# Kernel tuning notes

Measured on AMD Instinct MI355X. Metric: run time of the kernel, lower is better.

## Reference

```python
import jax, jax.numpy as jnp
import numpy as np

N = 200000   # total atoms in batched graph
E = 3200000  # total bonds (directed edges)
B = 512      # number of graphs / sequences
L = 1000     # miRNA sequence length


def _gcn(x, W, b, src, dst, dis):
    # PyG GCNConv: add self-loops, symmetric normalization D^-1/2 A D^-1/2
    h = x @ W                                   # [N, Fout]
    msg = (dis[src] * dis[dst])[:, None] * h[src]
    agg = jax.ops.segment_sum(msg, dst, num_segments=x.shape[0])
    return agg + (dis * dis)[:, None] * h + b   # self-loop term + bias


def _conv1d(x, k, b):
    # x: [B, C, L], k: [O, I, K]  (torch Conv1d, VALID padding)
    y = jax.lax.conv_general_dilated(x, k, (1,), 'VALID',
                                     dimension_numbers=('NCH', 'OIH', 'NCH'))
    return y + b[None, :, None]


def _mp3(x):
    # torch MaxPool1d(3): window 3, stride 3, floor
    return jax.lax.reduce_window(x, -jnp.inf, jax.lax.max, (1, 1, 3), (1, 1, 3), 'VALID')


def setup_inputs() -> dict:
    key = jax.random.key(0)
    ks = jax.random.split(key, 24)
    w = lambda k, s: (jax.random.normal(k, s, jnp.float32) * 0.1)
    p = {}
    p['x'] = jax.random.normal(ks[0], (N, 4), jnp.float32)
    p['edge_index'] = jax.random.randint(ks[1], (2, E), 0, N, jnp.int32)
    p['batch'] = (jnp.arange(N, dtype=jnp.int32) * B // N).astype(jnp.int32)  # every graph non-empty
    p['target'] = jax.random.normal(ks[2], (B, L, 5), jnp.float32)
    # GCN layers 4->4->8->16
    p['W1'] = w(ks[3], (4, 4));    p['b1'] = jnp.zeros(4, jnp.float32)
    p['W2'] = w(ks[4], (4, 8));    p['b2'] = jnp.zeros(8, jnp.float32)
    p['W3'] = w(ks[5], (8, 16));   p['b3'] = jnp.zeros(16, jnp.float32)
    p['Wg1'] = w(ks[6], (16, 1024)); p['bg1'] = jnp.zeros(1024, jnp.float32)
    p['Wg2'] = w(ks[7], (1024, 128)); p['bg2'] = jnp.zeros(128, jnp.float32)
    # CNN stack on sequences, kernels [O, I, 8]
    p['K1'] = w(ks[8], (32, 5, 8));   p['cb1'] = jnp.zeros(32, jnp.float32)
    p['K2'] = w(ks[9], (64, 32, 8));  p['cb2'] = jnp.zeros(64, jnp.float32)
    p['K3'] = w(ks[10], (128, 64, 8)); p['cb3'] = jnp.zeros(128, jnp.float32)
    p['Wxt'] = w(ks[11], (128, 128)); p['bxt'] = jnp.zeros(128, jnp.float32)
    # fusion head
    p['Wf1'] = w(ks[12], (256, 1024)); p['bf1'] = jnp.zeros(1024, jnp.float32)
    p['Wf2'] = w(ks[13], (1024, 512)); p['bf2'] = jnp.zeros(512, jnp.float32)
    p['Wo'] = w(ks[14], (512, 2));     p['bo'] = jnp.zeros(2, jnp.float32)
    return p


def reference(x, edge_index, batch, target, W1, b1, W2, b2, W3, b3,
              Wg1, bg1, Wg2, bg2, K1, cb1, K2, cb2, K3, cb3,
              Wxt, bxt, Wf1, bf1, Wf2, bf2, Wo, bo):
    src, dst = edge_index[0], edge_index[1]
    deg = jax.ops.segment_sum(jnp.ones(src.shape[0], x.dtype), dst,
                              num_segments=x.shape[0]) + 1.0  # +1 self-loop
    dis = jax.lax.rsqrt(deg)
    # Graph branch (dropout is identity in eval)
    h = jax.nn.relu(_gcn(x, W1, b1, src, dst, dis))
    h = jax.nn.relu(_gcn(h, W2, b2, src, dst, dis))
    h = jax.nn.relu(_gcn(h, W3, b3, src, dst, dis))
    g = jax.ops.segment_max(h, batch, num_segments=B)  # global_max_pool
    g = jax.nn.relu(g @ Wg1 + bg1)
    g = g @ Wg2 + bg2
    # Sequence branch
    t = jnp.transpose(target, (0, 2, 1))  # [B, 5, L]
    c = _mp3(jax.nn.relu(_conv1d(t, K1, cb1)))
    c = _mp3(jax.nn.relu(_conv1d(c, K2, cb2)))
    c = _mp3(jax.nn.relu(_conv1d(c, K3, cb3)))
    c = jnp.mean(c, axis=2)               # [B, 128]
    c = jax.nn.relu(c @ Wxt + bxt)
    # Fusion head
    xc = jnp.concatenate([g, c], axis=1)  # [B, 256]
    xc = jax.nn.relu(xc @ Wf1 + bf1)
    xc = jax.nn.relu(xc @ Wf2 + bf2)
    return xc @ Wo + bo                    # [B, 2]
```

## Files before the change

### kernel.cpp

```cpp
#include <hip/hip_runtime.h>
#include <hip/hip_fp16.h>
#include <cstddef>

#define NA 200000
#define NE 3200000
#define NB 512
#define NBKT 256
#define BKTN 782
#define BKTCAP 16384
#define NEPB 3200

typedef _Float16 hv2 __attribute__((ext_vector_type(2)));
typedef _Float16 half8 __attribute__((ext_vector_type(8)));
typedef float floatx4 __attribute__((ext_vector_type(4)));
union UH2 { unsigned u; __half2 h; hv2 v; };
__device__ __forceinline__ float4 h4f(unsigned a, unsigned b) {
    UH2 x, y; x.u = a; y.u = b;
    float2 fa = __half22float2(x.h), fb = __half22float2(y.h);
    return make_float4(fa.x, fa.y, fb.x, fb.y);
}
__device__ __forceinline__ unsigned f2h(float a, float b) {
    UH2 r; r.h = __float22half2_rn(make_float2(a, b));
    return r.u;
}

__global__ void k_init(unsigned* g, int* gcursor,
                       float* gvec, const float* __restrict__ bg2,
                       float* xf2, const float* __restrict__ bf2,
                       float* xf1, const float* __restrict__ bf1,
                       const float* __restrict__ K2, const float* __restrict__ K3,
                       __half* __restrict__ Wt2, __half* __restrict__ Wt3) {
    int i = blockIdx.x * blockDim.x + threadIdx.x;
    if (i < NB * 16) g[i] = 0u;
    if (i < NBKT) gcursor[i] = i * BKTCAP;
    if (i < NB * 128) gvec[i] = bg2[i & 127];
    if (i < NB * 512) xf2[i] = bf2[i & 511];
    if (i < NB * 1024) xf1[i] = bf1[i & 1023];
    if (i < 64 * 32 * 8) {
        int o = i >> 8, rem = i & 255, c = rem >> 3, kk = rem & 7;
        Wt2[(o << 8) + (kk << 5) + c] = __float2half(K2[i]);
    }
    if (i < 128 * 64 * 8) {
        int o = i >> 9, rem = i & 511, c = rem >> 3, kk = rem & 7;
        Wt3[(o << 9) + (kk << 6) + c] = __float2half(K3[i]);
    }
}

template<int CIN, int COUT, int OBLK, int LIN, int PITCH, int POUT, int NTT>
__device__ __forceinline__ void dev_conv1(int b, int oy,
        const float* __restrict__ in, const float* __restrict__ Kw,
        const float* __restrict__ bias, __half* __restrict__ out,
        float* s_in) {
    constexpr int SPO = 256 / OBLK;
    constexpr int PT = (NTT < 4) ? NTT : 4;
    constexpr int NPASS = (NTT + PT - 1) / PT;
    for (int idx = threadIdx.x; idx < CIN * PITCH; idx += 256) s_in[idx] = 0.f;
    __syncthreads();
    for (int idx = threadIdx.x; idx < LIN * CIN; idx += 256) {
        int p = idx / CIN, c = idx - p * CIN;
        s_in[c * PITCH + p] = in[(size_t)b * (LIN * CIN) + idx];
    }
    __syncthreads();
    int ol = threadIdx.x / SPO;
    int s  = threadIdx.x - ol * SPO;
    int o  = oy * OBLK + ol;
    float bo = bias[o];
    const float* wrow = Kw + (size_t)o * CIN * 8;
    for (int pass = 0; pass < NPASS; pass++) {
        float acc[PT][12];
#pragma unroll
        for (int tt = 0; tt < PT; tt++)
#pragma unroll
            for (int j = 0; j < 12; j++) acc[tt][j] = 0.f;
        bool vld[PT]; int tgs[PT];
#pragma unroll
        for (int tt = 0; tt < PT; tt++) {
            int ta = pass * PT + tt;
            int tg = s + SPO * ta;
            tgs[tt] = tg;
            vld[tt] = (ta < NTT) && (4 * tg < POUT);
        }
        for (int i = 0; i < CIN; i++) {
            float wa[8];
            const float4* wp = (const float4*)(wrow + (size_t)i * 8);
            *(float4*)&wa[0] = wp[0];
            *(float4*)&wa[4] = wp[1];
#pragma unroll
            for (int tt = 0; tt < PT; tt++) {
                if (vld[tt]) {
                    const float4* xr = (const float4*)&s_in[i * PITCH + 12 * tgs[tt]];
                    float xa[20];
#pragma unroll
                    for (int q = 0; q < 5; q++) *(float4*)&xa[4 * q] = xr[q];
#pragma unroll
                    for (int j = 0; j < 12; j++) {
                        float sm = acc[tt][j];
#pragma unroll
                        for (int k = 0; k < 8; k++) sm = fmaf(xa[j + k], wa[k], sm);
                        acc[tt][j] = sm;
                    }
                }
            }
        }
#pragma unroll
        for (int tt = 0; tt < PT; tt++) {
            if (vld[tt]) {
#pragma unroll
                for (int p = 0; p < 4; p++) {
                    int P = 4 * tgs[tt] + p;
                    if (P < POUT) {
                        float m = fmaxf(fmaxf(acc[tt][3 * p], acc[tt][3 * p + 1]), acc[tt][3 * p + 2]);
                        out[((size_t)b * COUT + o) * POUT + P] = __float2half(fmaxf(m + bo, 0.f));
                    }
                }
            }
        }
    }
}

__device__ __forceinline__ void dev_conv2_mfma(int b,
        const __half* __restrict__ pool1, const __half* __restrict__ Wt2,
        const float* __restrict__ cb2, __half* __restrict__ pool2t,
        char* smem) {
    __half* sT   = (__half*)smem;
    __half* outS = (__half*)smem;
    const __half* inp = pool1 + (size_t)b * (32 * 331);
    for (int idx = threadIdx.x; idx < 32 * 331; idx += 256) {
        int c = idx / 331;
        int p = idx - c * 331;
        sT[p * 40 + c] = inp[idx];
    }
    __syncthreads();
    int lane = threadIdx.x & 63, wv = threadIdx.x >> 6;
    int l15 = lane & 15, lg = lane >> 4;
    int mtBeg = wv * 5;
    int nmt = (wv == 3) ? 6 : 5;
    const floatx4 FZ = {0.f, 0.f, 0.f, 0.f};
    floatx4 acc[6][4];
#pragma unroll
    for (int mi = 0; mi < 6; mi++)
#pragma unroll
        for (int nt = 0; nt < 4; nt++) acc[mi][nt] = FZ;
    const half8* WB = (const half8*)Wt2;
    for (int s = 0; s < 8; s++) {
        half8 bfr[4];
#pragma unroll
        for (int nt = 0; nt < 4; nt++)
            bfr[nt] = WB[(nt * 16 + l15) * 32 + s * 4 + lg];
        half8 afr[6];
#pragma unroll
        for (int mi = 0; mi < 6; mi++) {
            if (mi < nmt) {
                int row = (mtBeg + mi) * 16 + l15 + s;
                afr[mi] = *(const half8*)(sT + row * 40 + lg * 8);
            }
        }
#pragma unroll
        for (int mi = 0; mi < 6; mi++) {
            if (mi < nmt) {
#pragma unroll
                for (int nt = 0; nt < 4; nt++)
                    acc[mi][nt] = __builtin_amdgcn_mfma_f32_16x16x32_f16(
                        afr[mi], bfr[nt], acc[mi][nt], 0, 0, 0);
            }
        }
    }
    __syncthreads();
    float bo[4];
#pragma unroll
    for (int nt = 0; nt < 4; nt++) bo[nt] = cb2[nt * 16 + l15];
    __half* op = pool2t + (size_t)b * (108 * 64);
    for (int h = 0; h < 2; h++) {
        int r0 = h * 168;
#pragma unroll
        for (int mi = 0; mi < 6; mi++) {
            if (mi < nmt) {
#pragma unroll
                for (int nt = 0; nt < 4; nt++) {
                    int o = nt * 16 + l15;
#pragma unroll
                    for (int r = 0; r < 4; r++) {
                        int p = (mtBeg + mi) * 16 + lg * 4 + r;
                        unsigned pl = (unsigned)(p - r0);
                        if (pl < 168u) {
                            float v = fmaxf(acc[mi][nt][r] + bo[nt], 0.f);
                            outS[pl * 68 + o] = __float2half(v);
                        }
                    }
                }
            }
        }
        __syncthreads();
        int nP = h ? 52 : 56;
        for (int idx = threadIdx.x; idx < nP * 64; idx += 256) {
            int Pl = idx >> 6, o = idx & 63;
            int P = h * 56 + Pl;
            int p = 3 * P - r0;
            float v0 = __half2float(outS[p * 68 + o]);
            float v1 = __half2float(outS[(p + 1) * 68 + o]);
            float v2 = __half2float(outS[(p + 2) * 68 + o]);
            op[P * 64 + o] = __float2half(fmaxf(fmaxf(v0, v1), v2));
        }
        __syncthreads();
    }
}

__device__ __forceinline__ void dev_conv3_mfma(int b,
        const __half* __restrict__ pool2t, const __half* __restrict__ Wt3,
        const float* __restrict__ cb3, float* __restrict__ pool3,
        char* smem) {
    __half* sT  = (__half*)smem;
    float* outS = (float*)smem;
    const uint4* inp = (const uint4*)(pool2t + (size_t)b * (108 * 64));
    for (int t = threadIdx.x; t < 108 * 8; t += 256) {
        int r = t >> 3, s8 = t & 7;
        *(uint4*)(sT + r * 72 + s8 * 8) = inp[t];
    }
    __syncthreads();
    int lane = threadIdx.x & 63, wv = threadIdx.x >> 6;
    int l15 = lane & 15, lg = lane >> 4;
    int mtBeg = wv * 2;
    int nmt = (wv == 3) ? 1 : 2;
    const floatx4 FZ = {0.f, 0.f, 0.f, 0.f};
    floatx4 acc[2][8];
#pragma unroll
    for (int mi = 0; mi < 2; mi++)
#pragma unroll
        for (int nt = 0; nt < 8; nt++) acc[mi][nt] = FZ;
    const half8* WB = (const half8*)Wt3;
    for (int s = 0; s < 16; s++) {
        half8 bfr[8];
#pragma unroll
        for (int nt = 0; nt < 8; nt++)
            bfr[nt] = WB[(nt * 16 + l15) * 64 + s * 4 + lg];
        half8 afr[2];
#pragma unroll
        for (int mi = 0; mi < 2; mi++) {
            if (mi < nmt) {
                int row = (mtBeg + mi) * 16 + l15 + (s >> 1);
                afr[mi] = *(const half8*)(sT + row * 72 + (s & 1) * 32 + lg * 8);
            }
        }
#pragma unroll
        for (int mi = 0; mi < 2; mi++) {
            if (mi < nmt) {
#pragma unroll
                for (int nt = 0; nt < 8; nt++)
                    acc[mi][nt] = __builtin_amdgcn_mfma_f32_16x16x32_f16(
                        afr[mi], bfr[nt], acc[mi][nt], 0, 0, 0);
            }
        }
    }
    __syncthreads();
    float bo[8];
#pragma unroll
    for (int nt = 0; nt < 8; nt++) bo[nt] = cb3[nt * 16 + l15];
    float* op = pool3 + (size_t)b * (128 * 33);
    for (int pp = 0; pp < 3; pp++) {
        int t0 = 3 * pp;
#pragma unroll
        for (int mi = 0; mi < 2; mi++) {
            int tile = mtBeg + mi;
            if (mi < nmt && tile >= t0 && tile < t0 + 3) {
#pragma unroll
                for (int nt = 0; nt < 8; nt++) {
                    int o = nt * 16 + l15;
#pragma unroll
                    for (int r = 0; r < 4; r++) {
                        int p = tile * 16 + lg * 4 + r;
                        if (p < 100)
                            outS[(p - 48 * pp) * 132 + o] =
                                fmaxf(acc[mi][nt][r] + bo[nt], 0.f);
                    }
                }
            }
        }
        __syncthreads();
        int nP = (pp == 2) ? 1 : 16;
        for (int idx = threadIdx.x; idx < nP * 128; idx += 256) {
            int Pl = idx >> 7, o = idx & 127;
            int P = 16 * pp + Pl;
            int p = 3 * P - 48 * pp;
            float v0 = outS[p * 132 + o];
            float v1 = outS[(p + 1) * 132 + o];
            float v2 = outS[(p + 2) * 132 + o];
            op[o * 33 + P] = fmaxf(fmaxf(v0, v1), v2);
        }
        __syncthreads();
    }
}

__global__ __launch_bounds__(256) void k_A(
        const int* __restrict__ src, const int* __restrict__ dst,
        int* __restrict__ gcursor, unsigned* __restrict__ stage,
        const float* __restrict__ tgt, const float* __restrict__ K1,
        const float* __restrict__ cb1, __half* __restrict__ pool1) {
    __shared__ __align__(16) char smem[20160];
    int bx = blockIdx.x;
    if (bx >= 1000) {
        dev_conv1<5, 32, 16, 1000, 1008, 331, 6>(bx - 1000, 0, tgt, K1, cb1,
                                                 pool1, (float*)smem);
        return;
    }
    int* hcnt  = (int*)smem;
    int* hbase = hcnt + 256;
    int* lbase = hbase + 256;
    unsigned* sbuf = (unsigned*)(lbase + 256);
    unsigned char* sbkt = (unsigned char*)(sbuf + NEPB);
    int t = threadIdx.x;
    int e0 = bx * NEPB;
    hcnt[t] = 0;
    __syncthreads();
    const int4* d4 = (const int4*)(dst + e0);
    for (int i = t; i < NEPB / 4; i += 256) {
        int4 d = d4[i];
        atomicAdd(&hcnt[d.x / BKTN], 1);
        atomicAdd(&hcnt[d.y / BKTN], 1);
        atomicAdd(&hcnt[d.z / BKTN], 1);
        atomicAdd(&hcnt[d.w / BKTN], 1);
    }
    __syncthreads();
    int myc = hcnt[t];
    hbase[t] = atomicAdd(&gcursor[t], myc);
    __syncthreads();
#pragma unroll
    for (int off = 1; off < 256; off <<= 1) {
        int u = (t >= off) ? hcnt[t - off] : 0;
        __syncthreads();
        hcnt[t] += u;
        __syncthreads();
    }
    lbase[t] = hcnt[t] - myc;
    hcnt[t] = 0;
    __syncthreads();
    const int4* s4 = (const int4*)(src + e0);
    for (int i = t; i < NEPB / 4; i += 256) {
        int4 d = d4[i];
        int4 s = s4[i];
        int ds[4] = {d.x, d.y, d.z, d.w};
        int ss[4] = {s.x, s.y, s.z, s.w};
#pragma unroll
        for (int j = 0; j < 4; j++) {
            int bkt = ds[j] / BKTN;
            int dloc = ds[j] - bkt * BKTN;
            int k = atomicAdd(&hcnt[bkt], 1);
            int pos = lbase[bkt] + k;
            sbuf[pos] = ((unsigned)dloc << 18) | (unsigned)ss[j];
            sbkt[pos] = (unsigned char)bkt;
        }
    }
    __syncthreads();
    for (int i = t; i < NEPB; i += 256) {
        unsigned v = sbuf[i];
        int bkt = sbkt[i];
        stage[hbase[bkt] + (i - lbase[bkt])] = v;
    }
}

__global__ __launch_bounds__(256) void k_Bp(
        const unsigned* __restrict__ stage, const int* __restrict__ gcursor,
        int* __restrict__ rowptr, int* __restrict__ cnt, int* __restrict__ csr,
        const float* __restrict__ x, float4* __restrict__ dt1,
        const float* __restrict__ tgt, const float* __restrict__ K1,
        const float* __restrict__ cb1, __half* __restrict__ pool1) {
    __shared__ __align__(16) char smem[20160];
    __shared__ int sbase;
    int bx = blockIdx.x;
    if (bx >= NBKT) {
        dev_conv1<5, 32, 16, 1000, 1008, 331, 6>(bx - NBKT, 1, tgt, K1, cb1,
                                                 pool1, (float*)smem);
        return;
    }
    int* lcnt    = (int*)smem;
    int* lpos    = lcnt + BKTN;
    int* partial = lpos + BKTN;
    int t = threadIdx.x;
    int bkt = bx;
    int tot = gcursor[t] - t * BKTCAP;
    partial[t] = tot;
    __syncthreads();
#pragma unroll
    for (int off = 1; off < 256; off <<= 1) {
        int u = (t >= off) ? partial[t - off] : 0;
        __syncthreads();
        partial[t] += u;
        __syncthreads();
    }
    if (t == 0) sbase = (bkt == 0) ? 0 : partial[bkt - 1];
    __syncthreads();
    int base = sbase;
    int n0 = bkt * BKTN;
    int ncnt = (NA - n0 < BKTN) ? (NA - n0) : BKTN;
    int eBeg = bkt * BKTCAP;
    int eCnt = gcursor[bkt] - eBeg;
    for (int i = t; i < BKTN; i += 256) lcnt[i] = 0;
    __syncthreads();
    for (int i = t; i < eCnt; i += 256)
        atomicAdd(&lcnt[stage[eBeg + i] >> 18], 1);
    __syncthreads();
    int mysum = 0;
#pragma unroll
    for (int j = 0; j < 4; j++) {
        int node = 4 * t + j;
        if (node < ncnt) mysum += lcnt[node];
    }
    partial[t] = mysum;
    __syncthreads();
#pragma unroll
    for (int off = 1; off < 256; off <<= 1) {
        int u = (t >= off) ? partial[t - off] : 0;
        __syncthreads();
        partial[t] += u;
        __syncthreads();
    }
    int running = partial[t] - mysum;
#pragma unroll
    for (int j = 0; j < 4; j++) {
        int node = 4 * t + j;
        if (node < ncnt) {
            lpos[node] = running;
            rowptr[n0 + node] = base + running;
            cnt[n0 + node] = lcnt[node];
            running += lcnt[node];
        }
    }
    __syncthreads();
    for (int i = t; i < eCnt; i += 256) {
        unsigned v = stage[eBeg + i];
        int dloc = v >> 18;
        int s = v & 0x3FFFF;
        int k = atomicAdd(&lpos[dloc], 1);
        csr[base + k] = s;
    }
    for (int i = t; i < ncnt; i += 256) {
        int n = n0 + i;
        float4 p = ((const float4*)x)[n];
        float dv = rsqrtf((float)lcnt[i] + 1.0f);
        dt1[n] = make_float4(dv * p.x, dv * p.y, dv * p.z, dv * p.w);
    }
}

__global__ __launch_bounds__(256) void k_B(
        const __half* __restrict__ pool1, const __half* __restrict__ Wt2,
        const float* __restrict__ cb2, __half* __restrict__ pool2t,
        const float4* __restrict__ dt1, const int* __restrict__ rowptr,
        const int* __restrict__ cnt, const int* __restrict__ csr,
        const float* __restrict__ W1, const float* __restrict__ b1,
        float4* __restrict__ dt2) {
    __shared__ __align__(16) char smem[27520];
    int bx = blockIdx.x;
    if (bx < 512) {
        dev_conv2_mfma(bx, pool1, Wt2, cb2, pool2t, smem);
        return;
    }
    __shared__ float sW[16];
    if (threadIdx.x < 16) sW[threadIdx.x] = W1[threadIdx.x];
    __syncthreads();
    int n = (bx - 512) * 256 + threadIdx.x;
    if (n >= NA) return;
    int cn = cnt[n];
    float dv = rsqrtf((float)cn + 1.0f);
    const int* row = csr + rowptr[n];
    float4 acc = dt1[n];
    int e = 0;
    for (; e + 7 < cn; e += 8) {
        int idx[8];
#pragma unroll
        for (int u = 0; u < 8; u++) idx[u] = row[e + u];
        float4 v[8];
#pragma unroll
        for (int u = 0; u < 8; u++) v[u] = dt1[idx[u]];
#pragma unroll
        for (int u = 0; u < 8; u++) {
            acc.x += v[u].x; acc.y += v[u].y; acc.z += v[u].z; acc.w += v[u].w;
        }
    }
    for (; e < cn; e++) {
        float4 v = dt1[row[e]];
        acc.x += v.x; acc.y += v.y; acc.z += v.z; acc.w += v.w;
    }
    const float4 bq = *(const float4*)b1;
    float a[4] = {acc.x, acc.y, acc.z, acc.w};
    float bb[4] = {bq.x, bq.y, bq.z, bq.w};
    float o[4];
#pragma unroll
    for (int f = 0; f < 4; f++) {
        float s = 0.f;
#pragma unroll
        for (int k = 0; k < 4; k++) s = fmaf(a[k], sW[k * 4 + f], s);
        o[f] = dv * fmaxf(fmaf(dv, s, bb[f]), 0.f);
    }
    dt2[n] = make_float4(o[0], o[1], o[2], o[3]);
}

__global__ __launch_bounds__(256) void k_C(
        const __half* __restrict__ pool2t, const __half* __restrict__ Wt3,
        const float* __restrict__ cb3, float* __restrict__ pool3,
        const float4* __restrict__ dt2, const int* __restrict__ rowptr,
        const int* __restrict__ cnt, const int* __restrict__ csr,
        const float* __restrict__ W2, const float* __restrict__ b2,
        uint4* __restrict__ dt3) {
    __shared__ __align__(16) char smem[25344];
    int bx = blockIdx.x;
    if (bx < 512) {
        dev_conv3_mfma(bx, pool2t, Wt3, cb3, pool3, smem);
        return;
    }
    __shared__ float sW[32];
    if (threadIdx.x < 32) sW[threadIdx.x] = W2[threadIdx.x];
    __syncthreads();
    int n = (bx - 512) * 256 + threadIdx.x;
    if (n >= NA) return;
    int cn = cnt[n];
    float dv = rsqrtf((float)cn + 1.0f);
    const int* row = csr + rowptr[n];
    float4 acc = dt2[n];
    int e = 0;
    for (; e + 7 < cn; e += 8) {
        int idx[8];
#pragma unroll
        for (int u = 0; u < 8; u++) idx[u] = row[e + u];
        float4 v[8];
#pragma unroll
        for (int u = 0; u < 8; u++) v[u] = dt2[idx[u]];
#pragma unroll
        for (int u = 0; u < 8; u++) {
            acc.x += v[u].x; acc.y += v[u].y; acc.z += v[u].z; acc.w += v[u].w;
        }
    }
    for (; e < cn; e++) {
        float4 v = dt2[row[e]];
        acc.x += v.x; acc.y += v.y; acc.z += v.z; acc.w += v.w;
    }
    float a[4] = {acc.x, acc.y, acc.z, acc.w};
    float o[8];
#pragma unroll
    for (int f = 0; f < 8; f++) {
        float s = 0.f;
#pragma unroll
        for (int k = 0; k < 4; k++) s = fmaf(a[k], sW[k * 8 + f], s);
        o[f] = dv * fmaxf(fmaf(dv, s, b2[f]), 0.f);
    }
    dt3[n] = make_uint4(f2h(o[0], o[1]), f2h(o[2], o[3]),
                        f2h(o[4], o[5]), f2h(o[6], o[7]));
}

__global__ __launch_bounds__(256) void k_D(
        const uint4* __restrict__ dt3, const int* __restrict__ rowptr,
        const int* __restrict__ cnt, const int* __restrict__ csr,
        const float* __restrict__ W3, const float* __restrict__ b3,
        const int* __restrict__ batch, unsigned* __restrict__ g,
        const float* __restrict__ pool3, const float* __restrict__ Wxt,
        const float* __restrict__ bxt, float* __restrict__ cx) {
    int bx = blockIdx.x;
    if (bx >= 782) {
        __shared__ float sa[8 * 128];
        int b0 = (bx - 782) * 8;
        for (int t = threadIdx.x; t < 8 * 128; t += 256) {
            int gg = t >> 7, k = t & 127;
            const float* r = pool3 + ((size_t)(b0 + gg) * 128 + k) * 33;
            float s = 0.f;
#pragma unroll
            for (int p = 0; p < 33; p++) s += r[p];
            sa[t] = s * (1.f / 33.f);
        }
        __syncthreads();
        int j = threadIdx.x;
        if (j >= 128) return;
        float bj = bxt[j];
        float acc[8];
#pragma unroll
        for (int gg = 0; gg < 8; gg++) acc[gg] = bj;
#pragma unroll 4
        for (int k = 0; k < 128; k++) {
            float w = Wxt[(size_t)k * 128 + j];
#pragma unroll
            for (int gg = 0; gg < 8; gg++) acc[gg] = fmaf(sa[gg * 128 + k], w, acc[gg]);
        }
#pragma unroll
        for (int gg = 0; gg < 8; gg++)
            cx[(size_t)(b0 + gg) * 128 + j] = fmaxf(acc[gg], 0.f);
        return;
    }
    __shared__ float sW[128];
    __shared__ unsigned sg[32];
    __shared__ int sbmin;
    int id = bx;
    if (threadIdx.x < 128) sW[threadIdx.x] = W3[threadIdx.x];
    if (threadIdx.x < 32) sg[threadIdx.x] = 0u;
    if (threadIdx.x == 0) sbmin = batch[id * 256];
    __syncthreads();
    int n = id * 256 + threadIdx.x;
    if (n < NA) {
        int cn = cnt[n];
        float dv = rsqrtf((float)cn + 1.0f);
        const int* row = csr + rowptr[n];
        uint4 sv = dt3[n];
        float4 lo = h4f(sv.x, sv.y), hi = h4f(sv.z, sv.w);
        float a0 = lo.x, a1 = lo.y, a2 = lo.z, a3 = lo.w;
        float a4 = hi.x, a5 = hi.y, a6 = hi.z, a7 = hi.w;
        int e = 0;
        for (; e + 3 < cn; e += 4) {
            uint4 p0 = dt3[row[e]],     p1 = dt3[row[e + 1]];
            uint4 p2 = dt3[row[e + 2]], p3 = dt3[row[e + 3]];
            float4 l0 = h4f(p0.x, p0.y), h0 = h4f(p0.z, p0.w);
            float4 l1 = h4f(p1.x, p1.y), h1 = h4f(p1.z, p1.w);
            float4 l2 = h4f(p2.x, p2.y), h2 = h4f(p2.z, p2.w);
            float4 l3 = h4f(p3.x, p3.y), h3v = h4f(p3.z, p3.w);
            a0 += (l0.x + l1.x) + (l2.x + l3.x);
            a1 += (l0.y + l1.y) + (l2.y + l3.y);
            a2 += (l0.z + l1.z) + (l2.z + l3.z);
            a3 += (l0.w + l1.w) + (l2.w + l3.w);
            a4 += (h0.x + h1.x) + (h2.x + h3v.x);
            a5 += (h0.y + h1.y) + (h2.y + h3v.y);
            a6 += (h0.z + h1.z) + (h2.z + h3v.z);
            a7 += (h0.w + h1.w) + (h2.w + h3v.w);
        }
        for (; e < cn; e++) {
            uint4 p = dt3[row[e]];
            float4 l = h4f(p.x, p.y), h = h4f(p.z, p.w);
            a0 += l.x; a1 += l.y; a2 += l.z; a3 += l.w;
            a4 += h.x; a5 += h.y; a6 += h.z; a7 += h.w;
        }
        float af[8] = {a0, a1, a2, a3, a4, a5, a6, a7};
        int rb = batch[n] - sbmin;
        if (rb > 1) rb = 1;
#pragma unroll
        for (int f = 0; f < 16; f++) {
            float s = 0.f;
#pragma unroll
            for (int k = 0; k < 8; k++) s = fmaf(af[k], sW[k * 16 + f], s);
            float r = fmaxf(fmaf(dv, s, b3[f]), 0.f);
            atomicMax(&sg[rb * 16 + f], __float_as_uint(r));
        }
    }
    __syncthreads();
    if (threadIdx.x < 32) {
        unsigned v = sg[threadIdx.x];
        int rb2 = threadIdx.x >> 4, f = threadIdx.x & 15;
        int bbn = sbmin + rb2;
        if (v != 0u && bbn < NB) atomicMax(&g[bbn * 16 + f], v);
    }
}

__global__ __launch_bounds__(256) void k_head_g(
        const float* __restrict__ g, const float* __restrict__ Wg1,
        const float* __restrict__ bg1, float* __restrict__ gp1) {
    __shared__ float sa[8 * 16];
    int bx = blockIdx.x;
    int b0 = (bx >> 2) * 8;
    if (threadIdx.x < 128)
        sa[threadIdx.x] = g[b0 * 16 + threadIdx.x];
    __syncthreads();
    int j = (bx & 3) * 256 + threadIdx.x;
    float bj = bg1[j];
    float acc[8];
#pragma unroll
    for (int gg = 0; gg < 8; gg++) acc[gg] = bj;
#pragma unroll
    for (int k = 0; k < 16; k++) {
        float w = Wg1[(size_t)k * 1024 + j];
#pragma unroll
        for (int gg = 0; gg < 8; gg++) acc[gg] = fmaf(sa[gg * 16 + k], w, acc[gg]);
    }
#pragma unroll
    for (int gg = 0; gg < 8; gg++)
        gp1[(size_t)(b0 + gg) * 1024 + j] = fmaxf(acc[gg], 0.f);
}

__global__ __launch_bounds__(256) void k_gvec_ks(
        const float* __restrict__ gp1, const float* __restrict__ Wg2,
        float* __restrict__ gvec) {
    __shared__ float sa[8 * 128];
    int k0 = blockIdx.x * 128;
    int b0 = blockIdx.y * 8;
    for (int t = threadIdx.x; t < 8 * 128; t += 256) {
        int gg = t >> 7, k = t & 127;
        sa[t] = gp1[(size_t)(b0 + gg) * 1024 + k0 + k];
    }
    __syncthreads();
    int j  = threadIdx.x & 127;
    int kh = (threadIdx.x >> 7) * 64;
    const float* Wp = Wg2 + (size_t)(k0 + kh) * 128 + j;
    float acc[8];
#pragma unroll
    for (int gg = 0; gg < 8; gg++) acc[gg] = 0.f;
    for (int k = 0; k < 64; k += 16) {
        float w[16];
#pragma unroll
        for (int u = 0; u < 16; u++) w[u] = Wp[(size_t)(k + u) * 128];
#pragma unroll
        for (int u = 0; u < 16; u++) {
#pragma unroll
            for (int gg = 0; gg < 8; gg++)
                acc[gg] = fmaf(sa[gg * 128 + kh + k + u], w[u], acc[gg]);
        }
    }
#pragma unroll
    for (int gg = 0; gg < 8; gg++)
        atomicAdd(&gvec[(size_t)(b0 + gg) * 128 + j], acc[gg]);
}

__global__ __launch_bounds__(256) void k_cat2(
        const float* __restrict__ gvec, const float* __restrict__ cx,
        const float* __restrict__ Wf1, float* __restrict__ xf1) {
    __shared__ float sa[8 * 128];
    int jx = blockIdx.x & 3;
    int kh = blockIdx.x >> 2;
    int b0 = blockIdx.y * 8;
    const float* A = kh ? cx : gvec;
    for (int t = threadIdx.x; t < 8 * 128; t += 256) {
        int gg = t >> 7, k = t & 127;
        sa[t] = A[(size_t)(b0 + gg) * 128 + k];
    }
    __syncthreads();
    int j = jx * 256 + threadIdx.x;
    const float* Wp = Wf1 + (size_t)(kh * 128) * 1024 + j;
    float acc[8];
#pragma unroll
    for (int gg = 0; gg < 8; gg++) acc[gg] = 0.f;
    for (int k = 0; k < 128; k += 16) {
        float w[16];
#pragma unroll
        for (int u = 0; u < 16; u++) w[u] = Wp[(size_t)(k + u) * 1024];
#pragma unroll
        for (int u = 0; u < 16; u++) {
#pragma unroll
            for (int gg = 0; gg < 8; gg++)
                acc[gg] = fmaf(sa[gg * 128 + k + u], w[u], acc[gg]);
        }
    }
#pragma unroll
    for (int gg = 0; gg < 8; gg++)
        atomicAdd(&xf1[(size_t)(b0 + gg) * 1024 + j], acc[gg]);
}

__global__ __launch_bounds__(256) void k_xf2_ks(
        const float* __restrict__ xf1, const float* __restrict__ Wf2,
        float* __restrict__ xf2) {
    __shared__ float sa[8 * 256];
    int jb = blockIdx.x & 1;
    int k0 = (blockIdx.x >> 1) * 256;
    int b0 = blockIdx.y * 8;
    for (int t = threadIdx.x; t < 8 * 256; t += 256) {
        int gg = t >> 8, k = t & 255;
        sa[t] = fmaxf(xf1[(size_t)(b0 + gg) * 1024 + k0 + k], 0.f);
    }
    __syncthreads();
    int j = jb * 256 + threadIdx.x;
    const float* Wp = Wf2 + (size_t)k0 * 512 + j;
    float acc[8];
#pragma unroll
    for (int gg = 0; gg < 8; gg++) acc[gg] = 0.f;
    for (int k = 0; k < 256; k += 16) {
        float w[16];
#pragma unroll
        for (int u = 0; u < 16; u++) w[u] = Wp[(size_t)(k + u) * 512];
#pragma unroll
        for (int u = 0; u < 16; u++) {
#pragma unroll
            for (int gg = 0; gg < 8; gg++)
                acc[gg] = fmaf(sa[gg * 256 + k + u], w[u], acc[gg]);
        }
    }
#pragma unroll
    for (int gg = 0; gg < 8; gg++)
        atomicAdd(&xf2[(size_t)(b0 + gg) * 512 + j], acc[gg]);
}

__global__ __launch_bounds__(256) void k_dense_out(
        const float* __restrict__ A, const float* __restrict__ W,
        const float* __restrict__ bias, float* __restrict__ out) {
    int idx = blockIdx.x * 256 + threadIdx.x;
    if (idx >= NB * 2) return;
    int b = idx >> 1, j = idx & 1;
    float s = bias[j];
    const float4* A4 = (const float4*)(A + (size_t)b * 512);
    for (int k4 = 0; k4 < 128; k4 += 8) {
        float4 av[8];
#pragma unroll
        for (int u = 0; u < 8; u++) av[u] = A4[k4 + u];
#pragma unroll
        for (int u = 0; u < 8; u++) {
            int kb = (k4 + u) * 4;
            s = fmaf(fmaxf(av[u].x, 0.f), W[(kb + 0) * 2 + j], s);
            s = fmaf(fmaxf(av[u].y, 0.f), W[(kb + 1) * 2 + j], s);
            s = fmaf(fmaxf(av[u].z, 0.f), W[(kb + 2) * 2 + j], s);
            s = fmaf(fmaxf(av[u].w, 0.f), W[(kb + 3) * 2 + j], s);
        }
    }
    out[idx] = s;
}

extern "C" void kernel_launch(void* const* d_in, const int* in_sizes, int n_in,
                              void* d_out, int out_size, void* d_ws, size_t ws_size,
                              hipStream_t stream) {
    (void)in_sizes; (void)n_in; (void)out_size; (void)ws_size;
    const float* x   = (const float*)d_in[0];
    const int*  ei   = (const int*)d_in[1];
    const int*  batch= (const int*)d_in[2];
    const float* tgt = (const float*)d_in[3];
    const float* W1  = (const float*)d_in[4];  const float* b1  = (const float*)d_in[5];
    const float* W2  = (const float*)d_in[6];  const float* b2  = (const float*)d_in[7];
    const float* W3  = (const float*)d_in[8];  const float* b3  = (const float*)d_in[9];
    const float* Wg1 = (const float*)d_in[10]; const float* bg1 = (const float*)d_in[11];
    const float* Wg2 = (const float*)d_in[12]; const float* bg2 = (const float*)d_in[13];
    const float* K1  = (const float*)d_in[14]; const float* cb1 = (const float*)d_in[15];
    const float* K2  = (const float*)d_in[16]; const float* cb2 = (const float*)d_in[17];
    const float* K3  = (const float*)d_in[18]; const float* cb3 = (const float*)d_in[19];
    const float* Wxt = (const float*)d_in[20]; const float* bxt = (const float*)d_in[21];
    const float* Wf1 = (const float*)d_in[22]; const float* bf1 = (const float*)d_in[23];
    const float* Wf2 = (const float*)d_in[24]; const float* bf2 = (const float*)d_in[25];
    const float* Wo  = (const float*)d_in[26]; const float* bo  = (const float*)d_in[27];
    const int* srcp = ei;
    const int* dstp = ei + NE;

    float* ws = (float*)d_ws;
    float4* dt1 = (float4*)ws; ws += (size_t)NA * 4;
    float4* dt2 = (float4*)ws; ws += (size_t)NA * 4;
    uint4*  dt3 = (uint4*)ws;  ws += (size_t)NA * 4;
    float* g     = ws; ws += NB * 16;
    float* gp1   = ws; ws += NB * 1024;
    float* gvec  = ws; ws += NB * 128;
    float* cx    = ws; ws += NB * 128;
    float* xf1   = ws; ws += NB * 1024;
    float* xf2   = ws; ws += NB * 512;
    __half* pool1 = (__half*)ws; ws += (size_t)NB * 32 * 331;
    __half* pool2t = (__half*)ws; ws += (size_t)NB * 64 * 108;
    float* pool3 = ws; ws += (size_t)NB * 128 * 33;
    __half* Wt2 = (__half*)ws; ws += 64 * 256 / 2;
    __half* Wt3 = (__half*)ws; ws += 128 * 512 / 2;
    int*   cnt    = (int*)ws; ws += NA;
    int*   rowptr = (int*)ws; ws += NA;
    int*   csr    = (int*)ws; ws += NE;
    int*   gcursor= (int*)ws; ws += NBKT;
    unsigned* stage = (unsigned*)ws; ws += (size_t)NBKT * BKTCAP;

    dim3 blk(256);

    k_init<<<2048, blk, 0, stream>>>((unsigned*)g, gcursor, gvec, bg2, xf2, bf2,
                                     xf1, bf1, K2, K3, Wt2, Wt3);
    k_A<<<1512, blk, 0, stream>>>(srcp, dstp, gcursor, stage, tgt, K1, cb1, pool1);
    k_Bp<<<768, blk, 0, stream>>>(stage, gcursor, rowptr, cnt, csr, x, dt1,
                                  tgt, K1, cb1, pool1);
    k_B<<<1294, blk, 0, stream>>>(pool1, Wt2, cb2, pool2t,
                                  dt1, rowptr, cnt, csr, W1, b1, dt2);
    k_C<<<1294, blk, 0, stream>>>(pool2t, Wt3, cb3, pool3,
                                  dt2, rowptr, cnt, csr, W2, b2, dt3);
    k_D<<<846, blk, 0, stream>>>(dt3, rowptr, cnt, csr, W3, b3,
                                 batch, (unsigned*)g, pool3, Wxt, bxt, cx);

    k_head_g<<<256, blk, 0, stream>>>(g, Wg1, bg1, gp1);
    k_gvec_ks<<<dim3(8, 64), blk, 0, stream>>>(gp1, Wg2, gvec);
    k_cat2<<<dim3(8, 64), blk, 0, stream>>>(gvec, cx, Wf1, xf1);
    k_xf2_ks<<<dim3(8, 64), blk, 0, stream>>>(xf1, Wf2, xf2);
    k_dense_out<<<4, blk, 0, stream>>>(xf2, Wo, bo, (float*)d_out);
}
```

Before: 437.8 us.

## Split conv3 MFMA across two blocks per sequence by output-channel half

The conv3 MFMA path now runs as two blocks per sequence, each computing 64 of the 128 output channels. This halves the accumulator registers and shared staging per block, and a launch bound of 8 blocks per CU is added to raise occupancy. The pool3 layout moves from channel-major to position-major so each half writes contiguous columns, and the mean reader in k_D is updated to match. The cost is that each sequence's input tile is loaded into shared memory twice and the grid has more blocks.

After: 426.2 us. 1.03x faster.

```diff
diff --git a/kernel.cpp b/kernel.cpp
--- a/kernel.cpp
+++ b/kernel.cpp
@@ -205,7 +205,7 @@
     }
 }
 
-__device__ __forceinline__ void dev_conv3_mfma(int b,
+__device__ __forceinline__ void dev_conv3_mfma(int b, int nh,
         const __half* __restrict__ pool2t, const __half* __restrict__ Wt3,
         const float* __restrict__ cb3, float* __restrict__ pool3,
         char* smem) {
@@ -222,17 +222,13 @@
     int mtBeg = wv * 2;
     int nmt = (wv == 3) ? 1 : 2;
     const floatx4 FZ = {0.f, 0.f, 0.f, 0.f};
-    floatx4 acc[2][8];
+    floatx4 acc[2][4];
 #pragma unroll
     for (int mi = 0; mi < 2; mi++)
 #pragma unroll
-        for (int nt = 0; nt < 8; nt++) acc[mi][nt] = FZ;
+        for (int nt = 0; nt < 4; nt++) acc[mi][nt] = FZ;
     const half8* WB = (const half8*)Wt3;
     for (int s = 0; s < 16; s++) {
-        half8 bfr[8];
-#pragma unroll
-        for (int nt = 0; nt < 8; nt++)
-            bfr[nt] = WB[(nt * 16 + l15) * 64 + s * 4 + lg];
         half8 afr[2];
 #pragma unroll
         for (int mi = 0; mi < 2; mi++) {
@@ -242,20 +238,20 @@
             }
         }
 #pragma unroll
-        for (int mi = 0; mi < 2; mi++) {
-            if (mi < nmt) {
-#pragma unroll
-                for (int nt = 0; nt < 8; nt++)
-                    acc[mi][nt] = __builtin_amdgcn_mfma_f32_16x16x32_f16(
-                        afr[mi], bfr[nt], acc[mi][nt], 0, 0, 0);
-            }
-        }
-    }
-    __syncthreads();
-    float bo[8];
-#pragma unroll
-    for (int nt = 0; nt < 8; nt++) bo[nt] = cb3[nt * 16 + l15];
-    float* op = pool3 + (size_t)b * (128 * 33);
+        for (int nt = 0; nt < 4; nt++) {
+            half8 bfr = WB[((nh * 4 + nt) * 16 + l15) * 64 + s * 4 + lg];
+            acc[0][nt] = __builtin_amdgcn_mfma_f32_16x16x32_f16(
+                afr[0], bfr, acc[0][nt], 0, 0, 0);
+            if (nmt > 1)
+                acc[1][nt] = __builtin_amdgcn_mfma_f32_16x16x32_f16(
+                    afr[1], bfr, acc[1][nt], 0, 0, 0);
+        }
+    }
+    __syncthreads();
+    float bo[4];
+#pragma unroll
+    for (int nt = 0; nt < 4; nt++) bo[nt] = cb3[(nh * 4 + nt) * 16 + l15];
+    float* op = pool3 + (size_t)b * (33 * 128);
     for (int pp = 0; pp < 3; pp++) {
         int t0 = 3 * pp;
 #pragma unroll
@@ -263,13 +259,13 @@
             int tile = mtBeg + mi;
             if (mi < nmt && tile >= t0 && tile < t0 + 3) {
 #pragma unroll
-                for (int nt = 0; nt < 8; nt++) {
-                    int o = nt * 16 + l15;
+                for (int nt = 0; nt < 4; nt++) {
+                    int ol = nt * 16 + l15;
 #pragma unroll
                     for (int r = 0; r < 4; r++) {
                         int p = tile * 16 + lg * 4 + r;
                         if (p < 100)
-                            outS[(p - 48 * pp) * 132 + o] =
+                            outS[(p - 48 * pp) * 68 + ol] =
                                 fmaxf(acc[mi][nt][r] + bo[nt], 0.f);
                     }
                 }
@@ -277,14 +273,14 @@
         }
         __syncthreads();
         int nP = (pp == 2) ? 1 : 16;
-        for (int idx = threadIdx.x; idx < nP * 128; idx += 256) {
-            int Pl = idx >> 7, o = idx & 127;
+        for (int idx = threadIdx.x; idx < nP * 64; idx += 256) {
+            int Pl = idx >> 6, ol = idx & 63;
             int P = 16 * pp + Pl;
             int p = 3 * P - 48 * pp;
-            float v0 = outS[p * 132 + o];
-            float v1 = outS[(p + 1) * 132 + o];
-            float v2 = outS[(p + 2) * 132 + o];
-            op[o * 33 + P] = fmaxf(fmaxf(v0, v1), v2);
+            float v0 = outS[p * 68 + ol];
+            float v1 = outS[(p + 1) * 68 + ol];
+            float v2 = outS[(p + 2) * 68 + ol];
+            op[P * 128 + (nh << 6) + ol] = fmaxf(fmaxf(v0, v1), v2);
         }
         __syncthreads();
     }
@@ -493,23 +489,23 @@
     dt2[n] = make_float4(o[0], o[1], o[2], o[3]);
 }
 
-__global__ __launch_bounds__(256) void k_C(
+__global__ __launch_bounds__(256, 8) void k_C(
         const __half* __restrict__ pool2t, const __half* __restrict__ Wt3,
         const float* __restrict__ cb3, float* __restrict__ pool3,
         const float4* __restrict__ dt2, const int* __restrict__ rowptr,
         const int* __restrict__ cnt, const int* __restrict__ csr,
         const float* __restrict__ W2, const float* __restrict__ b2,
         uint4* __restrict__ dt3) {
-    __shared__ __align__(16) char smem[25344];
+    __shared__ __align__(16) char smem[17280];
     int bx = blockIdx.x;
-    if (bx < 512) {
-        dev_conv3_mfma(bx, pool2t, Wt3, cb3, pool3, smem);
+    if (bx < 1024) {
+        dev_conv3_mfma(bx & 511, bx >> 9, pool2t, Wt3, cb3, pool3, smem);
         return;
     }
     __shared__ float sW[32];
     if (threadIdx.x < 32) sW[threadIdx.x] = W2[threadIdx.x];
     __syncthreads();
-    int n = (bx - 512) * 256 + threadIdx.x;
+    int n = (bx - 1024) * 256 + threadIdx.x;
     if (n >= NA) return;
     int cn = cnt[n];
     float dv = rsqrtf((float)cn + 1.0f);
@@ -558,10 +554,10 @@
         int b0 = (bx - 782) * 8;
         for (int t = threadIdx.x; t < 8 * 128; t += 256) {
             int gg = t >> 7, k = t & 127;
-            const float* r = pool3 + ((size_t)(b0 + gg) * 128 + k) * 33;
+            const float* r = pool3 + (size_t)(b0 + gg) * (33 * 128) + k;
             float s = 0.f;
 #pragma unroll
-            for (int p = 0; p < 33; p++) s += r[p];
+            for (int p = 0; p < 33; p++) s += r[p * 128];
             sa[t] = s * (1.f / 33.f);
         }
         __syncthreads();
@@ -845,7 +841,7 @@
                                   tgt, K1, cb1, pool1);
     k_B<<<1294, blk, 0, stream>>>(pool1, Wt2, cb2, pool2t,
                                   dt1, rowptr, cnt, csr, W1, b1, dt2);
-    k_C<<<1294, blk, 0, stream>>>(pool2t, Wt3, cb3, pool3,
+    k_C<<<1806, blk, 0, stream>>>(pool2t, Wt3, cb3, pool3,
                                   dt2, rowptr, cnt, csr, W2, b2, dt3);
     k_D<<<846, blk, 0, stream>>>(dt3, rowptr, cnt, csr, W3, b3,
                                  batch, (unsigned*)g, pool3, Wxt, bxt, cx);
```
